# Performance work log

Measured on AMD Instinct MI355X. Metric: run time of the kernel, lower is better.

Reference implementation:

```python
import jax, jax.numpy as jnp
import numpy as np

N_NODES = 100000
N_EDGES = 800000
D = 64
N_ITERS = 3  # n_layers - 1


def setup_inputs() -> dict:
    key = jax.random.key(0)
    k1, k2, k3, k4 = jax.random.split(key, 4)
    x = jax.random.normal(k1, (N_NODES, D), dtype=jnp.float32)
    edge_index = jax.random.randint(k2, (2, N_EDGES), 0, N_NODES, dtype=jnp.int64)
    edge_weight = jax.random.uniform(k3, (N_EDGES,), dtype=jnp.float32)
    # Linear(64, 64) weight, scaled ~ kaiming so 3 stacked layers stay bounded
    W = jax.random.normal(k4, (D, D), dtype=jnp.float32) * (1.0 / np.sqrt(D))
    b = jnp.zeros((D,), dtype=jnp.float32)
    return {"x": x, "edge_index": edge_index, "edge_weight": edge_weight, "W": W, "b": b}


def reference(x, edge_index, edge_weight, W, b):
    # Faithful math of RPINetEncoder.forward: (n_layers-1) iterations of
    # LinearAggregation (weighted scatter-add message passing + shared Linear)
    # followed by ReLU. Dropout output is discarded in the original -> no-op.
    src = edge_index[0]
    dst = edge_index[1]
    n = x.shape[0]
    for _ in range(N_ITERS):
        msgs = edge_weight[:, None] * x[src]                      # [E, D] gather
        agg = jax.ops.segment_sum(msgs, dst, num_segments=n)      # [N, D] scatter-add
        x = jax.nn.relu(agg @ W.T + b)                            # shared linear + relu
    return x
```

## Files before the change

### kernel.cpp

```cpp
#include <hip/hip_runtime.h>
#include <hip/hip_bf16.h>

#define D 64
#define FP_SCALE 262144.0f
#define FP_INV   (1.0f / 262144.0f)
#define NPC 32
#define LOG_NPC 5
#define ASTR 65

__device__ __forceinline__ unsigned short f2bf(float f) {
    unsigned int u = __float_as_uint(f);
    u += 0x7fffu + ((u >> 16) & 1u);
    return (unsigned short)(u >> 16);
}

__global__ void hist_kernel(const int* __restrict__ dst, int* __restrict__ chunkCnt, int E) {
    int e = blockIdx.x * blockDim.x + threadIdx.x;
    if (e < E) atomicAdd(&chunkCnt[dst[e] >> LOG_NPC], 1);
}

__global__ void scan_kernel(const int* __restrict__ chunkCnt, int* __restrict__ blockStart,
                            int* __restrict__ cursor, int nblk) {
    __shared__ int wsum[8];
    int t = threadIdx.x, lane = t & 63, w = t >> 6;
    int carry = 0;
    for (int base = 0; base < nblk; base += 512) {
        int i = base + t;
        int v = (i < nblk) ? chunkCnt[i] : 0;
        int incl = v;
        #pragma unroll
        for (int off = 1; off < 64; off <<= 1) {
            int x = __shfl_up(incl, off);
            if (lane >= off) incl += x;
        }
        if (lane == 63) wsum[w] = incl;
        __syncthreads();
        int wpre = 0;
        for (int j = 0; j < w; ++j) wpre += wsum[j];
        int tot = 0;
        for (int j = 0; j < 8; ++j) tot += wsum[j];
        if (i < nblk) {
            int st = carry + wpre + incl - v;
            blockStart[i] = st;
            cursor[i] = st;
        }
        carry += tot;
        __syncthreads();
    }
}

__global__ void fill_kernel(const int* __restrict__ src, const int* __restrict__ dst,
                            const float* __restrict__ ew, int* __restrict__ cursor,
                            unsigned long long* __restrict__ perm64, int E) {
    int e = blockIdx.x * blockDim.x + threadIdx.x;
    if (e < E) {
        int d = dst[e];
        int p = atomicAdd(&cursor[d >> LOG_NPC], 1);
        unsigned lo = ((unsigned)src[e] << LOG_NPC) | (unsigned)(d & (NPC - 1));
        perm64[p] = ((unsigned long long)__float_as_uint(ew[e] * FP_SCALE) << 32) | lo;
    }
}

template<bool IN_F32, bool OUT_BF>
__global__ void agg_fused_kernel(const void* __restrict__ xin,
                                 const unsigned long long* __restrict__ perm64,
                                 const int* __restrict__ blockStart,
                                 const float* __restrict__ W,
                                 const float* __restrict__ bias,
                                 void* __restrict__ xout,
                                 int N, int E) {
    __shared__ int acc[NPC * ASTR];
    __shared__ float Wt[D][D];
    __shared__ float bsh[D];
    int t = threadIdx.x;
    int bid = blockIdx.x;
    int nodeBase = bid * NPC;
    int nodeEnd = min(nodeBase + NPC, N);
    int es = blockStart[bid];
    int ee = (bid + 1 < (int)gridDim.x) ? blockStart[bid + 1] : E;

    for (int i = t; i < NPC * ASTR / 4; i += 256)
        reinterpret_cast<int4*>(acc)[i] = make_int4(0, 0, 0, 0);
    if (t < NPC * ASTR - (NPC * ASTR / 4) * 4)
        acc[(NPC * ASTR / 4) * 4 + t] = 0;
    for (int i = t; i < D * D; i += 256) {
        int j = i >> 6, d = i & 63;
        Wt[d][j] = W[i] * FP_INV;
    }
    if (t < D) bsh[t] = bias[t];
    __syncthreads();

    int g = t >> 4;
    int i16 = t & 15;
    int gl = g & 3;
    int w4 = g >> 2;

#define EDGE_ATOMIC(pk)                                                         \
    {                                                                           \
        unsigned lo_ = (unsigned)(pk);                                          \
        float w_ = __uint_as_float((unsigned)((pk) >> 32));                     \
        int slot_ = (int)(lo_ & (NPC - 1));                                     \
        int s_ = (int)(lo_ >> LOG_NPC);                                         \
        float v0_, v1_, v2_, v3_;                                               \
        if (IN_F32) {                                                           \
            float4 u_ = *reinterpret_cast<const float4*>(                       \
                (const float*)xin + (size_t)s_ * D + (i16 << 2));               \
            v0_ = u_.x; v1_ = u_.y; v2_ = u_.z; v3_ = u_.w;                     \
        } else {                                                                \
            uint2 u_ = *reinterpret_cast<const uint2*>(                         \
                (const unsigned short*)xin + (size_t)s_ * D + (i16 << 2));      \
            v0_ = __uint_as_float(u_.x << 16);                                  \
            v1_ = __uint_as_float(u_.x & 0xffff0000u);                          \
            v2_ = __uint_as_float(u_.y << 16);                                  \
            v3_ = __uint_as_float(u_.y & 0xffff0000u);                          \
        }                                                                       \
        int base_ = slot_ * ASTR + i16;                                         \
        atomicAdd(&acc[base_ +  0], (int)(w_ * v0_));                           \
        atomicAdd(&acc[base_ + 16], (int)(w_ * v1_));                           \
        atomicAdd(&acc[base_ + 32], (int)(w_ * v2_));                           \
        atomicAdd(&acc[base_ + 48], (int)(w_ * v3_));                           \
    }

    int cnt = ee - es;
    int qlen = (cnt + 3) >> 2;
    int qs = es + gl * qlen;
    int qe = min(qs + qlen, ee);
    for (int e = qs + w4 * 4; e < qe; e += 16) {
        int m = min(4, qe - e);
        if (m == 4) {
            unsigned long long pk0 = perm64[e + 0];
            unsigned long long pk1 = perm64[e + 1];
            unsigned long long pk2 = perm64[e + 2];
            unsigned long long pk3 = perm64[e + 3];
            EDGE_ATOMIC(pk0); EDGE_ATOMIC(pk1); EDGE_ATOMIC(pk2); EDGE_ATOMIC(pk3);
        } else {
            for (int r = 0; r < m; ++r) {
                unsigned long long pk = perm64[e + r];
                EDGE_ATOMIC(pk);
            }
        }
    }
#undef EDGE_ATOMIC
    __syncthreads();

    int wave = t >> 6, lane = t & 63;
    int sBase = wave * (NPC / 4);
    float o[NPC / 4];
    #pragma unroll
    for (int i = 0; i < NPC / 4; ++i) o[i] = 0.f;
    for (int q = 0; q < 16; ++q) {
        float w0 = Wt[4 * q + 0][lane];
        float w1 = Wt[4 * q + 1][lane];
        float w2 = Wt[4 * q + 2][lane];
        float w3 = Wt[4 * q + 3][lane];
        #pragma unroll
        for (int i = 0; i < NPC / 4; ++i) {
            int base = (sBase + i) * ASTR + q;
            float a0 = (float)acc[base +  0];
            float a1 = (float)acc[base + 16];
            float a2 = (float)acc[base + 32];
            float a3 = (float)acc[base + 48];
            o[i] = fmaf(a0, w0, fmaf(a1, w1, fmaf(a2, w2, fmaf(a3, w3, o[i]))));
        }
    }
    #pragma unroll
    for (int i = 0; i < NPC / 4; ++i) {
        int node = nodeBase + sBase + i;
        if (node < nodeEnd) {
            float v = fmaxf(bsh[lane] + o[i], 0.0f);
            size_t off = (size_t)node * D + lane;
            if (OUT_BF) ((unsigned short*)xout)[off] = f2bf(v);
            else        ((float*)xout)[off] = v;
        }
    }
}

__global__ void rpi_scatter_kernel(const float* __restrict__ x,
                                   const int* __restrict__ src,
                                   const int* __restrict__ dst,
                                   const float* __restrict__ ew,
                                   int* __restrict__ agg, int E) {
    int tid = blockIdx.x * blockDim.x + threadIdx.x;
    int e = tid >> 4;
    if (e >= E) return;
    int c = (tid & 15) << 2;
    int s = src[e], d = dst[e];
    float w = ew[e] * FP_SCALE;
    float4 v = *reinterpret_cast<const float4*>(&x[(size_t)s * D + c]);
    int* o = &agg[(size_t)d * D + c];
    atomicAdd(o + 0, (int)(w * v.x));
    atomicAdd(o + 1, (int)(w * v.y));
    atomicAdd(o + 2, (int)(w * v.z));
    atomicAdd(o + 3, (int)(w * v.w));
}

__global__ void rpi_linear_relu_kernel(const int* __restrict__ agg,
                                       const float* __restrict__ W,
                                       const float* __restrict__ b,
                                       float* __restrict__ out, int N) {
    __shared__ float Ws[D][D + 1];
    __shared__ float bs[D];
    int t = threadIdx.x;
    for (int i = t; i < D * D; i += 256) Ws[i >> 6][i & 63] = W[i];
    if (t < D) bs[t] = b[t];
    __syncthreads();
    int wave = t >> 6, lane = t & 63;
    int nwaves = gridDim.x * 4;
    for (int n = blockIdx.x * 4 + wave; n < N; n += nwaves) {
        const int* arow = &agg[(size_t)n * D];
        float acc = bs[lane];
        #pragma unroll
        for (int d = 0; d < D; ++d) acc = fmaf((float)arow[d] * FP_INV, Ws[lane][d], acc);
        out[(size_t)n * D + lane] = fmaxf(acc, 0.0f);
    }
}

extern "C" void kernel_launch(void* const* d_in, const int* in_sizes, int n_in,
                              void* d_out, int out_size, void* d_ws, size_t ws_size,
                              hipStream_t stream) {
    const float* x0 = (const float*)d_in[0];
    const int*   ei = (const int*)d_in[1];
    const float* ew = (const float*)d_in[2];
    const float* W  = (const float*)d_in[3];
    const float* b  = (const float*)d_in[4];
    float* out = (float*)d_out;

    int N = in_sizes[0] / D;
    int E = in_sizes[2];
    const int* src = ei;
    const int* dst = ei + E;

    int nblk = (N + NPC - 1) / NPC;
    size_t xeb = (size_t)N * D * sizeof(unsigned short);
    size_t off = 0;
    size_t o_xb1 = off; off += xeb;
    size_t o_xb2 = off; off += xeb;
    size_t o_p64 = off; off += (size_t)E * sizeof(unsigned long long);
    size_t o_cnt = off; off += (size_t)nblk * sizeof(int);
    size_t o_bs  = off; off += ((size_t)nblk + 2) * sizeof(int);
    size_t o_cur = off; off += ((size_t)nblk + 2) * sizeof(int);
    size_t need = off;

    if (ws_size >= need) {
        unsigned short* xb1 = (unsigned short*)((char*)d_ws + o_xb1);
        unsigned short* xb2 = (unsigned short*)((char*)d_ws + o_xb2);
        unsigned long long* perm64 = (unsigned long long*)((char*)d_ws + o_p64);
        int* chunkCnt   = (int*)((char*)d_ws + o_cnt);
        int* blockStart = (int*)((char*)d_ws + o_bs);
        int* cursor     = (int*)((char*)d_ws + o_cur);

        int eb = (E + 255) / 256;

        hipMemsetAsync(chunkCnt, 0, (size_t)nblk * sizeof(int), stream);
        hist_kernel<<<eb, 256, 0, stream>>>(dst, chunkCnt, E);
        scan_kernel<<<1, 512, 0, stream>>>(chunkCnt, blockStart, cursor, nblk);
        fill_kernel<<<eb, 256, 0, stream>>>(src, dst, ew, cursor, perm64, E);

        agg_fused_kernel<true,  true> <<<nblk, 256, 0, stream>>>(x0,  perm64, blockStart, W, b, xb2, N, E);
        agg_fused_kernel<false, true> <<<nblk, 256, 0, stream>>>(xb2, perm64, blockStart, W, b, xb1, N, E);
        agg_fused_kernel<false, false><<<nblk, 256, 0, stream>>>(xb1, perm64, blockStart, W, b, out, N, E);
    } else {
        int* agg = (int*)d_ws;
        const float* xcur = x0;
        int sb = (E * 16 + 255) / 256;
        for (int it = 0; it < 3; ++it) {
            hipMemsetAsync(agg, 0, (size_t)N * D * sizeof(int), stream);
            rpi_scatter_kernel<<<sb, 256, 0, stream>>>(xcur, src, dst, ew, agg, E);
            rpi_linear_relu_kernel<<<2048, 256, 0, stream>>>(agg, W, b, out, N);
            xcur = out;
        }
    }
}
```

Before: 358.8 us.

## Bucket edges per 4 destination nodes so each group owns its own edge range

Each block now covers 64 nodes instead of 32, and edges are bucketed by groups of 4 destination nodes (dst>>2) instead of by block. Each 16-lane group reads its own contiguous bucket range from a finer prefix scan rather than splitting the block's range into quarters. This is meant to localise LDS atomics to a few slots per group, reduce contention, and halve the block count. In exchange the single-block scan must cover 16x more buckets, groups with uneven in-degree become load-imbalanced, and the larger block needs more LDS and registers, which can lower occupancy.

```diff
diff --git a/kernel.cpp b/kernel.cpp
--- a/kernel.cpp
+++ b/kernel.cpp
@@ -4,8 +4,8 @@
 #define D 64
 #define FP_SCALE 262144.0f
 #define FP_INV   (1.0f / 262144.0f)
-#define NPC 32
-#define LOG_NPC 5
+#define NPC 64
+#define LOG_NPC 6
 #define ASTR 65
 
 __device__ __forceinline__ unsigned short f2bf(float f) {
@@ -14,19 +14,19 @@
     return (unsigned short)(u >> 16);
 }
 
-__global__ void hist_kernel(const int* __restrict__ dst, int* __restrict__ chunkCnt, int E) {
+__global__ void hist_kernel(const int* __restrict__ dst, int* __restrict__ bktCnt, int E) {
     int e = blockIdx.x * blockDim.x + threadIdx.x;
-    if (e < E) atomicAdd(&chunkCnt[dst[e] >> LOG_NPC], 1);
-}
-
-__global__ void scan_kernel(const int* __restrict__ chunkCnt, int* __restrict__ blockStart,
-                            int* __restrict__ cursor, int nblk) {
+    if (e < E) atomicAdd(&bktCnt[dst[e] >> 2], 1);
+}
+
+__global__ void scan_kernel(const int* __restrict__ bktCnt, int* __restrict__ bucketStart,
+                            int* __restrict__ cursor, int nbkt) {
     __shared__ int wsum[8];
     int t = threadIdx.x, lane = t & 63, w = t >> 6;
     int carry = 0;
-    for (int base = 0; base < nblk; base += 512) {
+    for (int base = 0; base < nbkt; base += 512) {
         int i = base + t;
-        int v = (i < nblk) ? chunkCnt[i] : 0;
+        int v = (i < nbkt) ? bktCnt[i] : 0;
         int incl = v;
         #pragma unroll
         for (int off = 1; off < 64; off <<= 1) {
@@ -39,14 +39,15 @@
         for (int j = 0; j < w; ++j) wpre += wsum[j];
         int tot = 0;
         for (int j = 0; j < 8; ++j) tot += wsum[j];
-        if (i < nblk) {
+        if (i < nbkt) {
             int st = carry + wpre + incl - v;
-            blockStart[i] = st;
+            bucketStart[i] = st;
             cursor[i] = st;
         }
         carry += tot;
         __syncthreads();
     }
+    if (t == 0) bucketStart[nbkt] = carry;
 }
 
 __global__ void fill_kernel(const int* __restrict__ src, const int* __restrict__ dst,
@@ -55,7 +56,7 @@
     int e = blockIdx.x * blockDim.x + threadIdx.x;
     if (e < E) {
         int d = dst[e];
-        int p = atomicAdd(&cursor[d >> LOG_NPC], 1);
+        int p = atomicAdd(&cursor[d >> 2], 1);
         unsigned lo = ((unsigned)src[e] << LOG_NPC) | (unsigned)(d & (NPC - 1));
         perm64[p] = ((unsigned long long)__float_as_uint(ew[e] * FP_SCALE) << 32) | lo;
     }
@@ -64,11 +65,11 @@
 template<bool IN_F32, bool OUT_BF>
 __global__ void agg_fused_kernel(const void* __restrict__ xin,
                                  const unsigned long long* __restrict__ perm64,
-                                 const int* __restrict__ blockStart,
+                                 const int* __restrict__ bucketStart,
                                  const float* __restrict__ W,
                                  const float* __restrict__ bias,
                                  void* __restrict__ xout,
-                                 int N, int E) {
+                                 int N) {
     __shared__ int acc[NPC * ASTR];
     __shared__ float Wt[D][D];
     __shared__ float bsh[D];
@@ -76,13 +77,9 @@
     int bid = blockIdx.x;
     int nodeBase = bid * NPC;
     int nodeEnd = min(nodeBase + NPC, N);
-    int es = blockStart[bid];
-    int ee = (bid + 1 < (int)gridDim.x) ? blockStart[bid + 1] : E;
 
     for (int i = t; i < NPC * ASTR / 4; i += 256)
         reinterpret_cast<int4*>(acc)[i] = make_int4(0, 0, 0, 0);
-    if (t < NPC * ASTR - (NPC * ASTR / 4) * 4)
-        acc[(NPC * ASTR / 4) * 4 + t] = 0;
     for (int i = t; i < D * D; i += 256) {
         int j = i >> 6, d = i & 63;
         Wt[d][j] = W[i] * FP_INV;
@@ -94,6 +91,7 @@
     int i16 = t & 15;
     int gl = g & 3;
     int w4 = g >> 2;
+    int r = gl * 4 + w4;
 
 #define EDGE_ATOMIC(pk)                                                         \
     {                                                                           \
@@ -121,40 +119,35 @@
         atomicAdd(&acc[base_ + 48], (int)(w_ * v3_));                           \
     }
 
-    int cnt = ee - es;
-    int qlen = (cnt + 3) >> 2;
-    int qs = es + gl * qlen;
-    int qe = min(qs + qlen, ee);
-    for (int e = qs + w4 * 4; e < qe; e += 16) {
-        int m = min(4, qe - e);
-        if (m == 4) {
-            unsigned long long pk0 = perm64[e + 0];
-            unsigned long long pk1 = perm64[e + 1];
-            unsigned long long pk2 = perm64[e + 2];
-            unsigned long long pk3 = perm64[e + 3];
-            EDGE_ATOMIC(pk0); EDGE_ATOMIC(pk1); EDGE_ATOMIC(pk2); EDGE_ATOMIC(pk3);
-        } else {
-            for (int r = 0; r < m; ++r) {
-                unsigned long long pk = perm64[e + r];
-                EDGE_ATOMIC(pk);
-            }
-        }
+    int bs0 = bucketStart[bid * 16 + r];
+    int bs1 = bucketStart[bid * 16 + r + 1];
+    int e = bs0;
+    for (; e + 4 <= bs1; e += 4) {
+        unsigned long long pk0 = perm64[e + 0];
+        unsigned long long pk1 = perm64[e + 1];
+        unsigned long long pk2 = perm64[e + 2];
+        unsigned long long pk3 = perm64[e + 3];
+        EDGE_ATOMIC(pk0); EDGE_ATOMIC(pk1); EDGE_ATOMIC(pk2); EDGE_ATOMIC(pk3);
+    }
+    for (; e < bs1; ++e) {
+        unsigned long long pk = perm64[e];
+        EDGE_ATOMIC(pk);
     }
 #undef EDGE_ATOMIC
     __syncthreads();
 
     int wave = t >> 6, lane = t & 63;
-    int sBase = wave * (NPC / 4);
-    float o[NPC / 4];
+    int sBase = wave * 16;
+    float o[16];
     #pragma unroll
-    for (int i = 0; i < NPC / 4; ++i) o[i] = 0.f;
+    for (int i = 0; i < 16; ++i) o[i] = 0.f;
     for (int q = 0; q < 16; ++q) {
         float w0 = Wt[4 * q + 0][lane];
         float w1 = Wt[4 * q + 1][lane];
         float w2 = Wt[4 * q + 2][lane];
         float w3 = Wt[4 * q + 3][lane];
         #pragma unroll
-        for (int i = 0; i < NPC / 4; ++i) {
+        for (int i = 0; i < 16; ++i) {
             int base = (sBase + i) * ASTR + q;
             float a0 = (float)acc[base +  0];
             float a1 = (float)acc[base + 16];
@@ -164,7 +157,7 @@
         }
     }
     #pragma unroll
-    for (int i = 0; i < NPC / 4; ++i) {
+    for (int i = 0; i < 16; ++i) {
         int node = nodeBase + sBase + i;
         if (node < nodeEnd) {
             float v = fmaxf(bsh[lane] + o[i], 0.0f);
@@ -231,34 +224,35 @@
     const int* dst = ei + E;
 
     int nblk = (N + NPC - 1) / NPC;
+    int nbkt = nblk * 16;
     size_t xeb = (size_t)N * D * sizeof(unsigned short);
     size_t off = 0;
     size_t o_xb1 = off; off += xeb;
     size_t o_xb2 = off; off += xeb;
     size_t o_p64 = off; off += (size_t)E * sizeof(unsigned long long);
-    size_t o_cnt = off; off += (size_t)nblk * sizeof(int);
-    size_t o_bs  = off; off += ((size_t)nblk + 2) * sizeof(int);
-    size_t o_cur = off; off += ((size_t)nblk + 2) * sizeof(int);
+    size_t o_cnt = off; off += (size_t)nbkt * sizeof(int);
+    size_t o_bs  = off; off += ((size_t)nbkt + 2) * sizeof(int);
+    size_t o_cur = off; off += ((size_t)nbkt + 2) * sizeof(int);
     size_t need = off;
 
     if (ws_size >= need) {
         unsigned short* xb1 = (unsigned short*)((char*)d_ws + o_xb1);
         unsigned short* xb2 = (unsigned short*)((char*)d_ws + o_xb2);
         unsigned long long* perm64 = (unsigned long long*)((char*)d_ws + o_p64);
-        int* chunkCnt   = (int*)((char*)d_ws + o_cnt);
-        int* blockStart = (int*)((char*)d_ws + o_bs);
-        int* cursor     = (int*)((char*)d_ws + o_cur);
+        int* bktCnt      = (int*)((char*)d_ws + o_cnt);
+        int* bucketStart = (int*)((char*)d_ws + o_bs);
+        int* cursor      = (int*)((char*)d_ws + o_cur);
 
         int eb = (E + 255) / 256;
 
-        hipMemsetAsync(chunkCnt, 0, (size_t)nblk * sizeof(int), stream);
-        hist_kernel<<<eb, 256, 0, stream>>>(dst, chunkCnt, E);
-        scan_kernel<<<1, 512, 0, stream>>>(chunkCnt, blockStart, cursor, nblk);
+        hipMemsetAsync(bktCnt, 0, (size_t)nbkt * sizeof(int), stream);
+        hist_kernel<<<eb, 256, 0, stream>>>(dst, bktCnt, E);
+        scan_kernel<<<1, 512, 0, stream>>>(bktCnt, bucketStart, cursor, nbkt);
         fill_kernel<<<eb, 256, 0, stream>>>(src, dst, ew, cursor, perm64, E);
 
-        agg_fused_kernel<true,  true> <<<nblk, 256, 0, stream>>>(x0,  perm64, blockStart, W, b, xb2, N, E);
-        agg_fused_kernel<false, true> <<<nblk, 256, 0, stream>>>(xb2, perm64, blockStart, W, b, xb1, N, E);
-        agg_fused_kernel<false, false><<<nblk, 256, 0, stream>>>(xb1, perm64, blockStart, W, b, out, N, E);
+        agg_fused_kernel<true,  true> <<<nblk, 256, 0, stream>>>(x0,  perm64, bucketStart, W, b, xb2, N);
+        agg_fused_kernel<false, true> <<<nblk, 256, 0, stream>>>(xb2, perm64, bucketStart, W, b, xb1, N);
+        agg_fused_kernel<false, false><<<nblk, 256, 0, stream>>>(xb1, perm64, bucketStart, W, b, out, N);
     } else {
         int* agg = (int*)d_ws;
         const float* xcur = x0;
```

Measured after the change: 366.4 us. +2.1%, slower.
